# Performance work log

Hardware: AMD Instinct MI355X
Metric: run time of the kernel (lower is better)

The kernel has to match this reference:

```python
import jax, jax.numpy as jnp
import numpy as np

N_NODES = 50000
N_EDGES = 1600000
IN_DIM = 128
HIDDEN = 256
N_CLASSES = 2
N_GRAPHS = 512
BN_EPS = 1e-5


def setup_inputs() -> dict:
    key = jax.random.key(0)
    ks = jax.random.split(key, 12)
    x = jax.random.normal(ks[0], (N_NODES, IN_DIM), dtype=jnp.float32)
    edge_index = jax.random.randint(ks[1], (2, N_EDGES), 0, N_NODES, dtype=jnp.int64)
    batch = jnp.sort(jax.random.randint(ks[2], (N_NODES,), 0, N_GRAPHS, dtype=jnp.int64))
    s1 = 1.0 / np.sqrt(IN_DIM)
    s2 = 1.0 / np.sqrt(HIDDEN)
    return {
        "x": x,
        "edge_index": edge_index,
        "batch": batch,
        # GIN MLP: Linear(in,hidden) -> BN -> ReLU -> Linear(hidden,hidden)
        "W1": jax.random.uniform(ks[3], (IN_DIM, HIDDEN), jnp.float32, -s1, s1),
        "b1": jnp.zeros((HIDDEN,), jnp.float32),
        "g1": jnp.ones((HIDDEN,), jnp.float32),
        "be1": jnp.zeros((HIDDEN,), jnp.float32),
        "W2": jax.random.uniform(ks[4], (HIDDEN, HIDDEN), jnp.float32, -s2, s2),
        "b2": jnp.zeros((HIDDEN,), jnp.float32),
        # attention gate: Linear(hidden, 1)
        "Wg": jax.random.uniform(ks[5], (HIDDEN, 1), jnp.float32, -s2, s2),
        "bg": jnp.zeros((1,), jnp.float32),
        # head: BN(hidden) -> Dropout(eval: identity) -> Linear(hidden, n_classes)
        "g2": jnp.ones((HIDDEN,), jnp.float32),
        "be2": jnp.zeros((HIDDEN,), jnp.float32),
        "Wh": jax.random.uniform(ks[6], (HIDDEN, N_CLASSES), jnp.float32, -s2, s2),
        "bh": jnp.zeros((N_CLASSES,), jnp.float32),
    }


def _batchnorm(h, gamma, beta):
    # training-mode BN: batch statistics over axis 0 (biased variance, as torch)
    mu = jnp.mean(h, axis=0)
    var = jnp.mean(jnp.square(h - mu), axis=0)
    return gamma * (h - mu) * jax.lax.rsqrt(var + BN_EPS) + beta


def reference(x, edge_index, batch, W1, b1, g1, be1, W2, b2, Wg, bg, g2, be2, Wh, bh):
    src, dst = edge_index[0], edge_index[1]
    # GINConv (eps=0): agg_i = sum_{j->i} x_j ; h = MLP(x + agg)
    agg = jax.ops.segment_sum(x[src], dst, num_segments=N_NODES)  # [N, in_dim]
    h = x + agg
    h = h @ W1 + b1                      # [N, hidden]
    h = jax.nn.relu(_batchnorm(h, g1, be1))
    h = h @ W2 + b2                      # [N, hidden]
    h = jax.nn.relu(h)                   # outer F.relu in forward
    # AttentionalAggregation: segment softmax of gate, weighted sum per graph
    gate = h @ Wg + bg                   # [N, 1]
    m = jax.ops.segment_max(gate, batch, num_segments=N_GRAPHS)  # [G, 1]
    e = jnp.exp(gate - m[batch])
    s = jax.ops.segment_sum(e, batch, num_segments=N_GRAPHS)     # [G, 1]
    alpha = e / s[batch]                 # [N, 1]
    pooled = jax.ops.segment_sum(alpha * h, batch, num_segments=N_GRAPHS)  # [G, hidden]
    # head: BN -> (Dropout eval = identity) -> Linear -> log_softmax
    z = _batchnorm(pooled, g2, be2) @ Wh + bh  # [G, n_classes]
    return jax.nn.log_softmax(z, axis=-1)
```

## Files before the change

### kernel.cpp

```cpp
#include <hip/hip_runtime.h>

typedef unsigned int u32;
typedef unsigned short ushort_t;
typedef __attribute__((ext_vector_type(8))) short bf16x8;
typedef __attribute__((ext_vector_type(4))) float f32x4;

__device__ __forceinline__ float bf2f_lo(u32 u){
  union{u32 i; float f;} v; v.i = u<<16; return v.f;
}
__device__ __forceinline__ float bf2f_hi(u32 u){
  union{u32 i; float f;} v; v.i = u & 0xFFFF0000u; return v.f;
}
__device__ __forceinline__ float bf2f_s(ushort_t u){
  union{u32 i; float f;} v; v.i = ((u32)u)<<16; return v.f;
}
__device__ __forceinline__ u32 pack2bf(float a, float b){
  union{float f; u32 i;} va, vb; va.f=a; vb.f=b;
  u32 ra = (va.i + 0x7FFF + ((va.i>>16)&1)) >> 16;
  u32 rb = (vb.i + 0x7FFF + ((vb.i>>16)&1)) & 0xFFFF0000u;
  return ra | rb;
}
__device__ __forceinline__ ushort_t f2bf1(float f){
  union{float f; u32 i;} v; v.f=f;
  u32 r = v.i + 0x7FFF + ((v.i>>16)&1);
  return (ushort_t)(r>>16);
}

__global__ __launch_bounds__(256) void to_bf16(const float* __restrict__ x, u32* __restrict__ xb, long n4){
  long i = (long)blockIdx.x*256 + threadIdx.x;
  if(i*4 >= n4*4) return;
  float4 v = ((const float4*)x)[i];
  uint2 o; o.x = pack2bf(v.x, v.y); o.y = pack2bf(v.z, v.w);
  ((uint2*)xb)[i] = o;
}

__global__ __launch_bounds__(256) void transpose_w(const float* __restrict__ W, ushort_t* __restrict__ Wt, int K){
  int n = blockIdx.x;
  for(int k = threadIdx.x; k < K; k += 256){
    Wt[(size_t)n*K + k] = f2bf1(W[(size_t)k*256 + n]);
  }
}

__global__ __launch_bounds__(256) void hist_k(const int* __restrict__ dst, int* __restrict__ bcount,
                                              int E, int N, int NB){
  __shared__ int h[1024];
  for(int i=threadIdx.x; i<1024; i+=256) h[i]=0;
  __syncthreads();
  int e0 = blockIdx.x*8192;
  int e1 = min(e0+8192, E);
  for(int i=e0+threadIdx.x; i<e1; i+=256){
    int d = dst[i];
    if((u32)d >= (u32)N) d = 0;
    atomicAdd(&h[d>>6], 1);
  }
  __syncthreads();
  for(int i=threadIdx.x; i<NB; i+=256){
    int v = h[i];
    if(v) atomicAdd(&bcount[i], v);
  }
}

__global__ __launch_bounds__(256) void bucket_scan(const int* __restrict__ bcount, int* __restrict__ bstart,
                                                   int* __restrict__ bcursor, int* __restrict__ offs,
                                                   int NB, int N, int E){
  __shared__ int tsum[256];
  int t = threadIdx.x;
  int base = t*4;
  int a0 = (base+0<NB)?bcount[base+0]:0;
  int a1 = (base+1<NB)?bcount[base+1]:0;
  int a2 = (base+2<NB)?bcount[base+2]:0;
  int a3 = (base+3<NB)?bcount[base+3]:0;
  int s0=a0, s1=s0+a1, s2=s1+a2, s3=s2+a3;
  tsum[t]=s3; __syncthreads();
  #pragma unroll
  for(int d=1; d<256; d<<=1){
    int v = (t>=d)?tsum[t-d]:0;
    __syncthreads();
    tsum[t]+=v;
    __syncthreads();
  }
  int prev = (t>0)?tsum[t-1]:0;
  if(base+0<NB){ bstart[base+0]=prev;    bcursor[(base+0)*16]=0; }
  if(base+1<NB){ bstart[base+1]=prev+s0; bcursor[(base+1)*16]=0; }
  if(base+2<NB){ bstart[base+2]=prev+s1; bcursor[(base+2)*16]=0; }
  if(base+3<NB){ bstart[base+3]=prev+s2; bcursor[(base+3)*16]=0; }
  if(t==255){ bstart[NB]=prev+s3; offs[N]=E; }
}

__global__ __launch_bounds__(256) void binscatter2(const int* __restrict__ src, const int* __restrict__ dst,
                                                   const int* __restrict__ bstart, int* __restrict__ bcursor,
                                                   u32* __restrict__ pairs, int E, int N, int NB){
  __shared__ int hist[1024];
  __shared__ int base[1024];
  int e0 = blockIdx.x*8192;
  int e1 = min(e0+8192, E);
  for(int i=threadIdx.x; i<NB; i+=256) hist[i]=0;
  __syncthreads();
  for(int i=e0+threadIdx.x; i<e1; i+=256){
    int d = dst[i];
    if((u32)d >= (u32)N) d = 0;
    atomicAdd(&hist[d>>6], 1);
  }
  __syncthreads();
  for(int i=threadIdx.x; i<NB; i+=256){
    int c = hist[i];
    base[i] = c ? (bstart[i] + atomicAdd(&bcursor[i*16], c)) : 0;
    hist[i] = 0;
  }
  __syncthreads();
  for(int i=e0+threadIdx.x; i<e1; i+=256){
    int d = dst[i]; if((u32)d >= (u32)N) d = 0;
    int s = src[i]; if((u32)s >= (u32)N) s = 0;
    int b = d>>6;
    int loc = atomicAdd(&hist[b], 1);
    pairs[base[b]+loc] = (u32)s | (((u32)(d & 63))<<17);
  }
}

__global__ __launch_bounds__(256) void bucket_csr(const u32* __restrict__ pairs, const int* __restrict__ bstart,
                                                  int* __restrict__ offs, int* __restrict__ elist, int N){
  __shared__ int dcnt[64];
  __shared__ int dcur[64];
  int b = blockIdx.x;
  int p0 = bstart[b], p1 = bstart[b+1];
  if(threadIdx.x < 64) dcnt[threadIdx.x] = 0;
  __syncthreads();
  for(int i=p0+threadIdx.x; i<p1; i+=256){
    u32 u = pairs[i];
    atomicAdd(&dcnt[u>>17], 1);
  }
  __syncthreads();
  if(threadIdx.x == 0){
    int running = p0;
    #pragma unroll
    for(int j=0;j<64;j++){
      dcur[j] = running;
      int node = b*64 + j;
      if(node < N) offs[node] = running;
      running += dcnt[j];
    }
  }
  __syncthreads();
  for(int i=p0+threadIdx.x; i<p1; i+=256){
    u32 u = pairs[i];
    int pos = atomicAdd(&dcur[u>>17], 1);
    elist[pos] = (int)(u & 0x1FFFFu);
  }
}

__global__ __launch_bounds__(256) void gather_sum_bf(const u32* __restrict__ xb, const int* __restrict__ offs,
                                                     const int* __restrict__ elist, u32* __restrict__ h0b,
                                                     int N, int E){
  int slot = threadIdx.x >> 4;
  int c = threadIdx.x & 15;
  int i = blockIdx.x*16 + slot;
  if(i >= N) return;
  const uint4* xr = (const uint4*)xb;
  uint4 xv = xr[(size_t)i*16 + c];
  float acc[8] = {
    bf2f_lo(xv.x), bf2f_hi(xv.x), bf2f_lo(xv.y), bf2f_hi(xv.y),
    bf2f_lo(xv.z), bf2f_hi(xv.z), bf2f_lo(xv.w), bf2f_hi(xv.w) };
  int e0 = offs[i], e1 = offs[i+1];
  e0 = max(0, min(e0, E));
  e1 = max(e0, min(e1, E));
  int j = e0;
  for(; j+4 <= e1; j += 4){
    int s0 = elist[j+0]; if((u32)s0 >= (u32)N) s0 = 0;
    int s1 = elist[j+1]; if((u32)s1 >= (u32)N) s1 = 0;
    int s2 = elist[j+2]; if((u32)s2 >= (u32)N) s2 = 0;
    int s3 = elist[j+3]; if((u32)s3 >= (u32)N) s3 = 0;
    uint4 v0 = xr[(size_t)s0*16 + c];
    uint4 v1 = xr[(size_t)s1*16 + c];
    uint4 v2 = xr[(size_t)s2*16 + c];
    uint4 v3 = xr[(size_t)s3*16 + c];
    acc[0]+=bf2f_lo(v0.x); acc[1]+=bf2f_hi(v0.x); acc[2]+=bf2f_lo(v0.y); acc[3]+=bf2f_hi(v0.y);
    acc[4]+=bf2f_lo(v0.z); acc[5]+=bf2f_hi(v0.z); acc[6]+=bf2f_lo(v0.w); acc[7]+=bf2f_hi(v0.w);
    acc[0]+=bf2f_lo(v1.x); acc[1]+=bf2f_hi(v1.x); acc[2]+=bf2f_lo(v1.y); acc[3]+=bf2f_hi(v1.y);
    acc[4]+=bf2f_lo(v1.z); acc[5]+=bf2f_hi(v1.z); acc[6]+=bf2f_lo(v1.w); acc[7]+=bf2f_hi(v1.w);
    acc[0]+=bf2f_lo(v2.x); acc[1]+=bf2f_hi(v2.x); acc[2]+=bf2f_lo(v2.y); acc[3]+=bf2f_hi(v2.y);
    acc[4]+=bf2f_lo(v2.z); acc[5]+=bf2f_hi(v2.z); acc[6]+=bf2f_lo(v2.w); acc[7]+=bf2f_hi(v2.w);
    acc[0]+=bf2f_lo(v3.x); acc[1]+=bf2f_hi(v3.x); acc[2]+=bf2f_lo(v3.y); acc[3]+=bf2f_hi(v3.y);
    acc[4]+=bf2f_lo(v3.z); acc[5]+=bf2f_hi(v3.z); acc[6]+=bf2f_lo(v3.w); acc[7]+=bf2f_hi(v3.w);
  }
  for(; j < e1; j++){
    int s = elist[j];
    if((u32)s >= (u32)N) s = 0;
    uint4 v = xr[(size_t)s*16 + c];
    acc[0]+=bf2f_lo(v.x); acc[1]+=bf2f_hi(v.x);
    acc[2]+=bf2f_lo(v.y); acc[3]+=bf2f_hi(v.y);
    acc[4]+=bf2f_lo(v.z); acc[5]+=bf2f_hi(v.z);
    acc[6]+=bf2f_lo(v.w); acc[7]+=bf2f_hi(v.w);
  }
  uint4 o;
  o.x = pack2bf(acc[0],acc[1]); o.y = pack2bf(acc[2],acc[3]);
  o.z = pack2bf(acc[4],acc[5]); o.w = pack2bf(acc[6],acc[7]);
  ((uint4*)h0b)[(size_t)i*16 + c] = o;
}

template<int K, bool BNA, bool RELUOUT, bool GATE, bool ABF16, bool OUTBF16>
__global__ __launch_bounds__(512) void gemm_mfma(const void* __restrict__ Ap, const ushort_t* __restrict__ Wt,
                                                 const float* __restrict__ bias,
                                                 const float* __restrict__ scale, const float* __restrict__ shift,
                                                 void* __restrict__ Cp, int M,
                                                 const float* __restrict__ Wg, const float* __restrict__ bg,
                                                 float* __restrict__ gate){
  __shared__ uint4 Al[8*128];
  __shared__ uint4 Bl[8*256];
  __shared__ float gacc[128];
  const int tid  = threadIdx.x;
  const int lane = tid & 63;
  const int wave = tid >> 6;
  const int lm   = lane & 15;
  const int q    = lane >> 4;
  const int mhalf= wave >> 2;
  const int nq   = wave & 3;
  const int m0   = blockIdx.x * 128;

  if(GATE && tid < 128) gacc[tid] = 0.f;

  f32x4 acc[4][4];
  #pragma unroll
  for(int i=0;i<4;i++)
    #pragma unroll
    for(int j=0;j<4;j++) acc[i][j] = (f32x4){0.f,0.f,0.f,0.f};

  for(int k0=0; k0<K; k0+=64){
    #pragma unroll
    for(int i=0;i<2;i++){
      int idx = tid*2 + i;
      int m = idx >> 3, c = idx & 7;
      int grow = m0 + m;
      int kk = k0 + c*8;
      uint4 v = make_uint4(0,0,0,0);
      if(ABF16){
        if(grow < M) v = *(const uint4*)((const ushort_t*)Ap + (size_t)grow*K + kk);
      } else {
        float4 u0 = make_float4(0,0,0,0), u1 = make_float4(0,0,0,0);
        if(grow < M){
          u0 = *(const float4*)((const float*)Ap + (size_t)grow*K + kk);
          u1 = *(const float4*)((const float*)Ap + (size_t)grow*K + kk + 4);
        }
        if(BNA){
          float4 s0 = *(const float4*)(scale+kk),  s1 = *(const float4*)(scale+kk+4);
          float4 t0 = *(const float4*)(shift+kk),  t1 = *(const float4*)(shift+kk+4);
          u0.x=fmaxf(fmaf(s0.x,u0.x,t0.x),0.f); u0.y=fmaxf(fmaf(s0.y,u0.y,t0.y),0.f);
          u0.z=fmaxf(fmaf(s0.z,u0.z,t0.z),0.f); u0.w=fmaxf(fmaf(s0.w,u0.w,t0.w),0.f);
          u1.x=fmaxf(fmaf(s1.x,u1.x,t1.x),0.f); u1.y=fmaxf(fmaf(s1.y,u1.y,t1.y),0.f);
          u1.z=fmaxf(fmaf(s1.z,u1.z,t1.z),0.f); u1.w=fmaxf(fmaf(s1.w,u1.w,t1.w),0.f);
        }
        v.x = pack2bf(u0.x,u0.y); v.y = pack2bf(u0.z,u0.w);
        v.z = pack2bf(u1.x,u1.y); v.w = pack2bf(u1.z,u1.w);
      }
      Al[c*128 + m] = v;
    }
    #pragma unroll
    for(int i=0;i<4;i++){
      int idx = tid*4 + i;
      int n = idx >> 3, c = idx & 7;
      Bl[c*256 + n] = *(const uint4*)(Wt + (size_t)n*K + k0 + c*8);
    }
    __syncthreads();
    #pragma unroll
    for(int ks=0; ks<2; ks++){
      int cc = ks*4 + q;
      bf16x8 af[4], bfr[4];
      #pragma unroll
      for(int mi=0; mi<4; mi++)
        af[mi] = *((const bf16x8*)&Al[cc*128 + mhalf*64 + mi*16 + lm]);
      #pragma unroll
      for(int ni=0; ni<4; ni++)
        bfr[ni] = *((const bf16x8*)&Bl[cc*256 + nq*64 + ni*16 + lm]);
      #pragma unroll
      for(int mi=0; mi<4; mi++)
        #pragma unroll
        for(int ni=0; ni<4; ni++)
          acc[mi][ni] = __builtin_amdgcn_mfma_f32_16x16x32_bf16(af[mi], bfr[ni], acc[mi][ni], 0, 0, 0);
    }
    __syncthreads();
  }

  float bb[4], wgv[4];
  #pragma unroll
  for(int ni=0; ni<4; ni++){
    int col = nq*64 + ni*16 + lm;
    bb[ni] = bias[col];
    if(GATE) wgv[ni] = Wg[col];
  }
  #pragma unroll
  for(int mi=0; mi<4; mi++){
    int rowloc0 = mhalf*64 + mi*16 + q*4;
    float gp[4] = {0.f,0.f,0.f,0.f};
    #pragma unroll
    for(int ni=0; ni<4; ni++){
      int col = nq*64 + ni*16 + lm;
      f32x4 o = acc[mi][ni];
      #pragma unroll
      for(int r=0; r<4; r++){
        float v = o[r] + bb[ni];
        if(RELUOUT) v = fmaxf(v, 0.f);
        int row = m0 + rowloc0 + r;
        if(row < M){
          if(OUTBF16) ((ushort_t*)Cp)[(size_t)row*256 + col] = f2bf1(v);
          else        ((float*)Cp)[(size_t)row*256 + col] = v;
        }
        if(GATE) gp[r] = fmaf(v, wgv[ni], gp[r]);
      }
    }
    if(GATE){
      #pragma unroll
      for(int r=0; r<4; r++){
        if(m0 + rowloc0 + r < M) atomicAdd(&gacc[rowloc0 + r], gp[r]);
      }
    }
  }
  if(GATE){
    __syncthreads();
    if(tid < 128){
      int row = m0 + tid;
      if(row < M) gate[row] = gacc[tid] + bg[0];
    }
  }
}

__global__ __launch_bounds__(256) void col_stats2(const float* __restrict__ h, float* __restrict__ psum,
                                                  float* __restrict__ pq, int M, int rpb, int nblk){
  int b = blockIdx.x;
  int g = threadIdx.x >> 6;
  int lane = threadIdx.x & 63;
  int c0 = lane*4;
  int r0 = b*rpb;
  int r1 = min(r0+rpb, M);
  float4 s4 = make_float4(0.f,0.f,0.f,0.f);
  float4 q4 = make_float4(0.f,0.f,0.f,0.f);
  for(int r=r0+g; r<r1; r+=4){
    float4 v = *(const float4*)(h + (size_t)r*256 + c0);
    s4.x+=v.x; s4.y+=v.y; s4.z+=v.z; s4.w+=v.w;
    q4.x=fmaf(v.x,v.x,q4.x); q4.y=fmaf(v.y,v.y,q4.y);
    q4.z=fmaf(v.z,v.z,q4.z); q4.w=fmaf(v.w,v.w,q4.w);
  }
  __shared__ float ls[1024];
  __shared__ float lq[1024];
  *(float4*)&ls[g*256+c0] = s4;
  *(float4*)&lq[g*256+c0] = q4;
  __syncthreads();
  if(threadIdx.x < 64){
    #pragma unroll
    for(int j=0;j<4;j++){
      int c = c0+j;
      float s = ls[c]+ls[256+c]+ls[512+c]+ls[768+c];
      float q = lq[c]+lq[256+c]+lq[512+c]+lq[768+c];
      psum[(size_t)c*nblk + b] = s;
      pq[(size_t)c*nblk + b]   = q;
    }
  }
}

__global__ __launch_bounds__(512) void stats_fin(const float* __restrict__ psum, const float* __restrict__ pq,
                                                 const float* __restrict__ gamma, const float* __restrict__ beta,
                                                 float* __restrict__ scale, float* __restrict__ shift,
                                                 int nblk, float invM){
  __shared__ float red[512];
  int t = threadIdx.x;
  const float* src = (t<256) ? (psum + (size_t)t*nblk) : (pq + (size_t)(t-256)*nblk);
  float s = 0.f;
  for(int i=0;i<nblk;i+=4){
    float4 v = *(const float4*)(src+i);
    s += v.x+v.y+v.z+v.w;
  }
  red[t]=s; __syncthreads();
  if(t<256){
    float mu  = red[t]*invM;
    float var = fmaxf(red[256+t]*invM - mu*mu, 0.f);
    float sc  = gamma[t] * rsqrtf(var + 1e-5f);
    scale[t]=sc; shift[t]=fmaf(-mu, sc, beta[t]);
  }
}

__global__ __launch_bounds__(256) void pool_k(const ushort_t* __restrict__ h2b, const float* __restrict__ gate,
                                              const int* __restrict__ batch, float* __restrict__ pooled, int N){
  int g = blockIdx.x;
  __shared__ int sb[2];
  __shared__ float red[4];
  __shared__ float s_m, s_inv;
  if(threadIdx.x < 2){
    int target = g + threadIdx.x;
    int lo=0, hi=N;
    while(lo<hi){ int mid=(lo+hi)>>1; if(batch[mid] < target) lo=mid+1; else hi=mid; }
    sb[threadIdx.x] = lo;
  }
  __syncthreads();
  int beg = sb[0], end = sb[1];
  float mx = -1e30f;
  for(int i=beg+threadIdx.x; i<end; i+=256) mx = fmaxf(mx, gate[i]);
  #pragma unroll
  for(int d=32; d>0; d>>=1) mx = fmaxf(mx, __shfl_down(mx, d, 64));
  if((threadIdx.x&63)==0) red[threadIdx.x>>6] = mx;
  __syncthreads();
  if(threadIdx.x==0) s_m = fmaxf(fmaxf(red[0],red[1]), fmaxf(red[2],red[3]));
  __syncthreads();
  float m = s_m;
  float s = 0.f;
  for(int i=beg+threadIdx.x; i<end; i+=256) s += expf(gate[i]-m);
  #pragma unroll
  for(int d=32; d>0; d>>=1) s += __shfl_down(s, d, 64);
  if((threadIdx.x&63)==0) red[threadIdx.x>>6] = s;
  __syncthreads();
  if(threadIdx.x==0){
    float tot = red[0]+red[1]+red[2]+red[3];
    s_inv = (tot > 0.f) ? 1.f/tot : 0.f;
  }
  __syncthreads();
  float inv = s_inv;
  int t = threadIdx.x;
  float acc = 0.f;
  int i = beg;
  for(; i+2 <= end; i += 2){
    float a0 = expf(gate[i]-m) * inv;
    float a1 = expf(gate[i+1]-m) * inv;
    float h0 = bf2f_s(h2b[(size_t)i*256 + t]);
    float h1 = bf2f_s(h2b[(size_t)(i+1)*256 + t]);
    acc = fmaf(a0, h0, acc);
    acc = fmaf(a1, h1, acc);
  }
  for(; i < end; i++){
    float a = expf(gate[i]-m) * inv;
    acc = fmaf(a, bf2f_s(h2b[(size_t)i*256 + t]), acc);
  }
  pooled[g*256 + t] = acc;
}

__global__ __launch_bounds__(256) void head_k(const float* __restrict__ pooled,
                                              const float* __restrict__ sc2, const float* __restrict__ sh2,
                                              const float* __restrict__ Wh, const float* __restrict__ bh,
                                              float* __restrict__ out, int G){
  int w = (blockIdx.x*256 + threadIdx.x) >> 6;
  int l = threadIdx.x & 63;
  if(w >= G) return;
  float4 v  = *(const float4*)(pooled + (size_t)w*256 + l*4);
  float4 sc = *(const float4*)(sc2 + l*4);
  float4 sh = *(const float4*)(sh2 + l*4);
  float vv[4] = { fmaf(sc.x,v.x,sh.x), fmaf(sc.y,v.y,sh.y), fmaf(sc.z,v.z,sh.z), fmaf(sc.w,v.w,sh.w) };
  float4 w0 = *(const float4*)(Wh + (size_t)l*8);
  float4 w1 = *(const float4*)(Wh + (size_t)l*8 + 4);
  float a0 = vv[0]*w0.x + vv[1]*w0.z + vv[2]*w1.x + vv[3]*w1.z;
  float a1 = vv[0]*w0.y + vv[1]*w0.w + vv[2]*w1.y + vv[3]*w1.w;
  #pragma unroll
  for(int d=32; d>0; d>>=1){ a0 += __shfl_down(a0,d,64); a1 += __shfl_down(a1,d,64); }
  if(l==0){
    float z0 = a0 + bh[0];
    float z1 = a1 + bh[1];
    float mz = fmaxf(z0,z1);
    float lse = mz + logf(expf(z0-mz) + expf(z1-mz));
    out[w*2]   = z0 - lse;
    out[w*2+1] = z1 - lse;
  }
}

extern "C" void kernel_launch(void* const* d_in, const int* in_sizes, int n_in,
                              void* d_out, int out_size, void* d_ws, size_t ws_size,
                              hipStream_t stream){
  const float* x   = (const float*)d_in[0];
  const int*   ei  = (const int*)d_in[1];
  const int*   bat = (const int*)d_in[2];
  const float* W1  = (const float*)d_in[3];
  const float* b1  = (const float*)d_in[4];
  const float* g1  = (const float*)d_in[5];
  const float* be1 = (const float*)d_in[6];
  const float* W2  = (const float*)d_in[7];
  const float* b2  = (const float*)d_in[8];
  const float* Wg  = (const float*)d_in[9];
  const float* bg  = (const float*)d_in[10];
  const float* g2  = (const float*)d_in[11];
  const float* be2 = (const float*)d_in[12];
  const float* Wh  = (const float*)d_in[13];
  const float* bh  = (const float*)d_in[14];

  const int N = in_sizes[0] / 128;
  const int E = in_sizes[1] / 2;
  const int G = out_size / 2;
  const int NB = (N + 63) >> 6;
  const int NBLK1 = 512;
  const int NBLK2 = 64;

  char* ws = (char*)d_ws;
  u32*   h0b    = (u32*)ws;
  u32*   xb     = (u32*)(ws + 12800000);
  int*   elist  = (int*)(ws + 25600000);
  u32*   pairs  = (u32*)(ws + 32000000);
  int*   offs   = (int*)(ws + 38400000);
  int*   bcount = (int*)(ws + 38600192);
  int*   bstart = (int*)(ws + 38604288);
  int*   bcursor= (int*)(ws + 38608640);
  ushort_t* h2b = (ushort_t*)ws;
  float* h1     = (float*)(ws + 51200000);
  char*  p2 = ws + 102400000;
  float* psum1 = (float*)p2;          p2 += 256*NBLK1*4;
  float* pq1   = (float*)p2;          p2 += 256*NBLK1*4;
  float* psum2 = (float*)p2;          p2 += 256*NBLK2*4;
  float* pq2   = (float*)p2;          p2 += 256*NBLK2*4;
  float* sc1   = (float*)p2;          p2 += 1024;
  float* sh1   = (float*)p2;          p2 += 1024;
  float* gate  = (float*)p2;          p2 += (size_t)N*4 + 256;
  float* pooled= (float*)p2;          p2 += (size_t)G*256*4;
  float* sc2   = (float*)p2;          p2 += 1024;
  float* sh2   = (float*)p2;          p2 += 1024;
  ushort_t* W1t = (ushort_t*)p2;      p2 += 256*128*2;
  ushort_t* W2t = (ushort_t*)p2;      p2 += 256*256*2;

  const int* src = ei;
  const int* dst = ei + E;

  hipMemsetAsync(bcount, 0, (size_t)NB*4, stream);

  transpose_w<<<256, 256, 0, stream>>>(W1, W1t, 128);
  transpose_w<<<256, 256, 0, stream>>>(W2, W2t, 256);
  long n4 = (long)N*128/4;
  to_bf16    <<<(int)((n4+255)/256), 256, 0, stream>>>(x, xb, n4);

  int nchunk = (E + 8191)/8192;
  hist_k     <<<nchunk, 256, 0, stream>>>(dst, bcount, E, N, NB);
  bucket_scan<<<1, 256, 0, stream>>>(bcount, bstart, bcursor, offs, NB, N, E);
  binscatter2<<<nchunk, 256, 0, stream>>>(src, dst, bstart, bcursor, pairs, E, N, NB);
  bucket_csr <<<NB, 256, 0, stream>>>(pairs, bstart, offs, elist, N);
  gather_sum_bf<<<(N+15)/16, 256, 0, stream>>>(xb, offs, elist, h0b, N, E);

  int gblocks = (N + 127)/128;
  gemm_mfma<128,false,false,false,true,false><<<gblocks, 512, 0, stream>>>(
      h0b, W1t, b1, nullptr, nullptr, h1, N, nullptr, nullptr, nullptr);
  int rpb1 = (N + NBLK1 - 1)/NBLK1;
  col_stats2 <<<NBLK1, 256, 0, stream>>>(h1, psum1, pq1, N, rpb1, NBLK1);
  stats_fin  <<<1, 512, 0, stream>>>(psum1, pq1, g1, be1, sc1, sh1, NBLK1, 1.0f/(float)N);
  gemm_mfma<256,true,true,true,false,true><<<gblocks, 512, 0, stream>>>(
      h1, W2t, b2, sc1, sh1, h2b, N, Wg, bg, gate);

  pool_k <<<G, 256, 0, stream>>>(h2b, gate, bat, pooled, N);
  int rpb2 = (G + NBLK2 - 1)/NBLK2;
  col_stats2 <<<NBLK2, 256, 0, stream>>>(pooled, psum2, pq2, G, rpb2, NBLK2);
  stats_fin  <<<1, 512, 0, stream>>>(psum2, pq2, g2, be2, sc2, sh2, NBLK2, 1.0f/(float)G);
  head_k <<<(G+3)/4, 256, 0, stream>>>(pooled, sc2, sh2, Wh, bh, (float*)d_out, G);
}
```

Before: 371.9 us.

## Store first GEMM output as bf16 and pad LDS tiles against bank conflicts

```diff
diff --git a/kernel.cpp b/kernel.cpp
--- a/kernel.cpp
+++ b/kernel.cpp
@@ -204,8 +204,8 @@
                                                  void* __restrict__ Cp, int M,
                                                  const float* __restrict__ Wg, const float* __restrict__ bg,
                                                  float* __restrict__ gate){
-  __shared__ uint4 Al[8*128];
-  __shared__ uint4 Bl[8*256];
+  __shared__ uint4 Al[8*129];
+  __shared__ uint4 Bl[8*257];
   __shared__ float gacc[128];
   const int tid  = threadIdx.x;
   const int lane = tid & 63;
@@ -234,6 +234,18 @@
       uint4 v = make_uint4(0,0,0,0);
       if(ABF16){
         if(grow < M) v = *(const uint4*)((const ushort_t*)Ap + (size_t)grow*K + kk);
+        if(BNA){
+          float f0=bf2f_lo(v.x), f1=bf2f_hi(v.x), f2=bf2f_lo(v.y), f3=bf2f_hi(v.y);
+          float f4=bf2f_lo(v.z), f5=bf2f_hi(v.z), f6=bf2f_lo(v.w), f7=bf2f_hi(v.w);
+          float4 s0 = *(const float4*)(scale+kk),  s1 = *(const float4*)(scale+kk+4);
+          float4 t0 = *(const float4*)(shift+kk),  t1 = *(const float4*)(shift+kk+4);
+          f0=fmaxf(fmaf(s0.x,f0,t0.x),0.f); f1=fmaxf(fmaf(s0.y,f1,t0.y),0.f);
+          f2=fmaxf(fmaf(s0.z,f2,t0.z),0.f); f3=fmaxf(fmaf(s0.w,f3,t0.w),0.f);
+          f4=fmaxf(fmaf(s1.x,f4,t1.x),0.f); f5=fmaxf(fmaf(s1.y,f5,t1.y),0.f);
+          f6=fmaxf(fmaf(s1.z,f6,t1.z),0.f); f7=fmaxf(fmaf(s1.w,f7,t1.w),0.f);
+          v.x = pack2bf(f0,f1); v.y = pack2bf(f2,f3);
+          v.z = pack2bf(f4,f5); v.w = pack2bf(f6,f7);
+        }
       } else {
         float4 u0 = make_float4(0,0,0,0), u1 = make_float4(0,0,0,0);
         if(grow < M){
@@ -251,13 +263,13 @@
         v.x = pack2bf(u0.x,u0.y); v.y = pack2bf(u0.z,u0.w);
         v.z = pack2bf(u1.x,u1.y); v.w = pack2bf(u1.z,u1.w);
       }
-      Al[c*128 + m] = v;
+      Al[c*129 + m] = v;
     }
     #pragma unroll
     for(int i=0;i<4;i++){
       int idx = tid*4 + i;
       int n = idx >> 3, c = idx & 7;
-      Bl[c*256 + n] = *(const uint4*)(Wt + (size_t)n*K + k0 + c*8);
+      Bl[c*257 + n] = *(const uint4*)(Wt + (size_t)n*K + k0 + c*8);
     }
     __syncthreads();
     #pragma unroll
@@ -266,10 +278,10 @@
       bf16x8 af[4], bfr[4];
       #pragma unroll
       for(int mi=0; mi<4; mi++)
-        af[mi] = *((const bf16x8*)&Al[cc*128 + mhalf*64 + mi*16 + lm]);
+        af[mi] = *((const bf16x8*)&Al[cc*129 + mhalf*64 + mi*16 + lm]);
       #pragma unroll
       for(int ni=0; ni<4; ni++)
-        bfr[ni] = *((const bf16x8*)&Bl[cc*256 + nq*64 + ni*16 + lm]);
+        bfr[ni] = *((const bf16x8*)&Bl[cc*257 + nq*64 + ni*16 + lm]);
       #pragma unroll
       for(int mi=0; mi<4; mi++)
         #pragma unroll
@@ -318,6 +330,40 @@
     if(tid < 128){
       int row = m0 + tid;
       if(row < M) gate[row] = gacc[tid] + bg[0];
+    }
+  }
+}
+
+__global__ __launch_bounds__(256) void col_stats_bf(const u32* __restrict__ h, float* __restrict__ psum,
+                                                    float* __restrict__ pq, int M, int rpb, int nblk){
+  int b = blockIdx.x;
+  int g = threadIdx.x >> 6;
+  int lane = threadIdx.x & 63;
+  int c0 = lane*4;
+  int r0 = b*rpb;
+  int r1 = min(r0+rpb, M);
+  float4 s4 = make_float4(0.f,0.f,0.f,0.f);
+  float4 q4 = make_float4(0.f,0.f,0.f,0.f);
+  for(int r=r0+g; r<r1; r+=4){
+    uint2 u = *(const uint2*)(h + (size_t)r*128 + lane*2);
+    float v0=bf2f_lo(u.x), v1=bf2f_hi(u.x), v2=bf2f_lo(u.y), v3=bf2f_hi(u.y);
+    s4.x+=v0; s4.y+=v1; s4.z+=v2; s4.w+=v3;
+    q4.x=fmaf(v0,v0,q4.x); q4.y=fmaf(v1,v1,q4.y);
+    q4.z=fmaf(v2,v2,q4.z); q4.w=fmaf(v3,v3,q4.w);
+  }
+  __shared__ float ls[1024];
+  __shared__ float lq[1024];
+  *(float4*)&ls[g*256+c0] = s4;
+  *(float4*)&lq[g*256+c0] = q4;
+  __syncthreads();
+  if(threadIdx.x < 64){
+    #pragma unroll
+    for(int j=0;j<4;j++){
+      int c = c0+j;
+      float s = ls[c]+ls[256+c]+ls[512+c]+ls[768+c];
+      float q = lq[c]+lq[256+c]+lq[512+c]+lq[768+c];
+      psum[(size_t)c*nblk + b] = s;
+      pq[(size_t)c*nblk + b]   = q;
     }
   }
 }
@@ -492,7 +538,7 @@
   int*   bstart = (int*)(ws + 38604288);
   int*   bcursor= (int*)(ws + 38608640);
   ushort_t* h2b = (ushort_t*)ws;
-  float* h1     = (float*)(ws + 51200000);
+  u32*   h1b    = (u32*)(ws + 51200000);
   char*  p2 = ws + 102400000;
   float* psum1 = (float*)p2;          p2 += 256*NBLK1*4;
   float* pq1   = (float*)p2;          p2 += 256*NBLK1*4;
@@ -525,13 +571,13 @@
   gather_sum_bf<<<(N+15)/16, 256, 0, stream>>>(xb, offs, elist, h0b, N, E);
 
   int gblocks = (N + 127)/128;
-  gemm_mfma<128,false,false,false,true,false><<<gblocks, 512, 0, stream>>>(
-      h0b, W1t, b1, nullptr, nullptr, h1, N, nullptr, nullptr, nullptr);
+  gemm_mfma<128,false,false,false,true,true><<<gblocks, 512, 0, stream>>>(
+      h0b, W1t, b1, nullptr, nullptr, h1b, N, nullptr, nullptr, nullptr);
   int rpb1 = (N + NBLK1 - 1)/NBLK1;
-  col_stats2 <<<NBLK1, 256, 0, stream>>>(h1, psum1, pq1, N, rpb1, NBLK1);
+  col_stats_bf <<<NBLK1, 256, 0, stream>>>(h1b, psum1, pq1, N, rpb1, NBLK1);
   stats_fin  <<<1, 512, 0, stream>>>(psum1, pq1, g1, be1, sc1, sh1, NBLK1, 1.0f/(float)N);
-  gemm_mfma<256,true,true,true,false,true><<<gblocks, 512, 0, stream>>>(
-      h1, W2t, b2, sc1, sh1, h2b, N, Wg, bg, gate);
+  gemm_mfma<256,true,true,true,true,true><<<gblocks, 512, 0, stream>>>(
+      h1b, W2t, b2, sc1, sh1, h2b, N, Wg, bg, gate);
 
   pool_k <<<G, 256, 0, stream>>>(h2b, gate, bat, pooled, N);
   int rpb2 = (G + NBLK2 - 1)/NBLK2;
```

New measurement: 362.9 us. 1.02x faster.
